# Kernel optimization log

Hardware: AMD Instinct MI355X
Metric: run time of the kernel (lower is better)

The kernel has to match this reference:

```python
import jax, jax.numpy as jnp
import numpy as np
import math

WS = 11
SIGMA = 1.5

def _gaussian_window(ws=WS, sigma=SIGMA):
    i = np.arange(ws)
    g = np.exp(-((i - ws // 2) ** 2) / (2.0 * sigma ** 2))
    g = (g / g.sum()).astype(np.float32)
    w2d = np.outer(g, g)  # [ws, ws]
    return jnp.asarray(w2d)

def _depthwise_conv(x, win2d):
    # x: [B, C, H, W]; win2d: [ws, ws]
    C = x.shape[1]
    kernel = jnp.broadcast_to(win2d[None, None], (C, 1, WS, WS)).astype(x.dtype)  # [C,1,ws,ws]
    return jax.lax.conv_general_dilated(
        x, kernel,
        window_strides=(1, 1),
        padding=[(WS // 2, WS // 2), (WS // 2, WS // 2)],
        dimension_numbers=("NCHW", "OIHW", "NCHW"),
        feature_group_count=C,
    )

def setup_inputs() -> dict:
    key = jax.random.key(0)
    k1, k2, k3 = jax.random.split(key, 3)
    B, C, H, W = 16, 3, 512, 512
    x = jax.random.uniform(k1, (B, C, H, W), dtype=jnp.float32)
    y = jax.random.uniform(k2, (B, C, H, W), dtype=jnp.float32)
    conf = jax.random.uniform(k3, (B, 1, H, W), dtype=jnp.float32)
    return {"x": x, "y": y, "conf": conf}

def reference(x, y, conf):
    win2d = _gaussian_window()
    mu_x = _depthwise_conv(x, win2d)
    mu_y = _depthwise_conv(y, win2d)
    mu_x2, mu_y2, mu_xy = mu_x * mu_x, mu_y * mu_y, mu_x * mu_y
    sigma_x2 = _depthwise_conv(x * x, win2d) - mu_x2
    sigma_y2 = _depthwise_conv(y * y, win2d) - mu_y2
    sigma_xy = _depthwise_conv(x * y, win2d) - mu_xy
    C1, C2 = 0.01 ** 2, 0.03 ** 2
    ssim = (2 * mu_xy + C1) * (2 * sigma_xy + C2) / ((mu_x2 + mu_y2 + C1) * (sigma_x2 + sigma_y2 + C2))
    loss_map = jnp.clip(1.0 - ssim, 0.0, 1.0)
    loss_map = loss_map * conf  # broadcast over channels
    return jnp.mean(loss_map)
```

## Files before the change

### kernel.cpp

```cpp
#include <hip/hip_runtime.h>
#include <cmath>

#define TW 32
#define SUB 32
#define NSUB 2
#define TH (SUB * NSUB)
#define HR (SUB + 10)
#define NT 256
#define IMG 512
#define SSIM_C1 1e-4f
#define SSIM_C2 9e-4f

struct GaussWin { float g[11]; };

typedef float v2f __attribute__((ext_vector_type(2)));

__device__ __forceinline__ v2f pk_fma(v2f a, v2f b, v2f c) {
    return __builtin_elementwise_fma(a, b, c);
}

__device__ __forceinline__ void h_pass_rows(const float* __restrict__ xp,
                                            const float* __restrict__ yp,
                                            int tx0, int gy0, int slot0, int nrows,
                                            const v2f* __restrict__ w2,
                                            float4* __restrict__ s_h, int tid) {
    constexpr int WI[11] = {0,1,2,3,4,5,4,3,2,1,0};
    if (tid < nrows * 4) {
        const int r = tid >> 2;
        const int cs = (tid & 3) * 8;
        const int gy = gy0 + r;
        const int slot = slot0 + r;
        const float* xrow = xp + gy * IMG;
        const float* yrow = yp + gy * IMG;
        const int c0 = tx0 + cs - 8;

        const bool fast = ((unsigned)gy < IMG) & ((unsigned)c0 <= (unsigned)(IMG - 24));

        float4 fx[6], fy[6];
        if (fast) {
            #pragma unroll
            for (int q = 0; q < 6; q++) {
                fx[q] = *(const float4*)(xrow + c0 + 4 * q);
                fy[q] = *(const float4*)(yrow + c0 + 4 * q);
            }
        } else {
            const bool rowok = ((unsigned)gy < IMG);
            #pragma unroll
            for (int q = 0; q < 6; q++) {
                int col = c0 + 4 * q;
                fx[q] = make_float4(0.f, 0.f, 0.f, 0.f);
                fy[q] = make_float4(0.f, 0.f, 0.f, 0.f);
                if (rowok && (unsigned)col <= (unsigned)(IMG - 4)) {
                    fx[q] = *(const float4*)(xrow + col);
                    fy[q] = *(const float4*)(yrow + col);
                }
            }
        }
        float vxa[24], vya[24];
        #pragma unroll
        for (int q = 0; q < 6; q++) {
            vxa[4*q+0]=fx[q].x; vxa[4*q+1]=fx[q].y; vxa[4*q+2]=fx[q].z; vxa[4*q+3]=fx[q].w;
            vya[4*q+0]=fy[q].x; vya[4*q+1]=fy[q].y; vya[4*q+2]=fy[q].z; vya[4*q+3]=fy[q].w;
        }

        v2f amu[8], a2[8];
        #pragma unroll
        for (int j = 0; j < 8; j++) { amu[j]=(v2f){0.f,0.f}; a2[j]=(v2f){0.f,0.f}; }
        #pragma unroll
        for (int k = 0; k < 18; k++) {
            float xv = vxa[k + 3], yv = vya[k + 3];
            v2f xy = (v2f){xv, yv};
            v2f p2 = xy * xy;
            v2f zw = (v2f){p2.x + p2.y, xv * yv};
            const int jlo = (k - 10 > 0) ? (k - 10) : 0;
            const int jhi = (k < 7) ? k : 7;
            #pragma unroll
            for (int j = jlo; j <= jhi; j++) {
                v2f w = w2[WI[k - j]];
                amu[j] = pk_fma(xy, w, amu[j]);
                a2[j]  = pk_fma(zw, w, a2[j]);
            }
        }
        const int quad = cs & 24;
        const int base0 = cs + 2 * (cs >> 3) + 5 * slot;
        #pragma unroll
        for (int j = 0; j < 8; j++) {
            int pc = quad | ((base0 + j) & 7);
            s_h[slot * TW + pc] = make_float4(amu[j].x, amu[j].y, a2[j].x, a2[j].y);
        }
    }
}

__launch_bounds__(NT, 4)
__global__ void ssim_tile_kernel(const float* __restrict__ x,
                                 const float* __restrict__ y,
                                 const float* __restrict__ conf,
                                 float* __restrict__ partials,
                                 float* __restrict__ out,
                                 int use_ws, float scale,
                                 GaussWin W) {
    __shared__ float4 s_h[HR * TW];
    __shared__ float  s_red[4];

    const int tid = threadIdx.x;
    const int plane = blockIdx.z;
    const int tx0 = blockIdx.x * TW;
    const int ty0 = blockIdx.y * TH;
    const float* xp = x + plane * (IMG * IMG);
    const float* yp = y + plane * (IMG * IMG);
    const int cbase = (plane / 3) * (IMG * IMG);

    constexpr int WI[11] = {0,1,2,3,4,5,4,3,2,1,0};
    v2f w2[6];
    #pragma unroll
    for (int i = 0; i < 6; i++) w2[i] = (v2f){W.g[i], W.g[i]};

    const int c   = tid & 31;
    const int r0c = (tid >> 5) * 4;
    const int cquad = c & 24;
    const int cb0 = c + 2 * (c >> 3) + 5 * r0c;
    int bidx[8];
    #pragma unroll
    for (int p = 0; p < 8; p++) {
        bidx[p] = r0c * TW + (cquad | ((cb0 + 5 * p) & 7));
    }

    float lsum = 0.f;
    float4 st0, st1;

    #pragma unroll
    for (int s = 0; s < NSUB; s++) {
        if (s == 0) {
            h_pass_rows(xp, yp, tx0, ty0 - 5, 0, HR, w2, s_h, tid);
        } else {
            __syncthreads();
            ((float4*)s_h)[tid] = st0;
            if (tid < 64) ((float4*)s_h)[256 + tid] = st1;
            h_pass_rows(xp, yp, tx0, ty0 + SUB * s + 5, 10, SUB, w2, s_h, tid);
        }

        float cf[4];
        #pragma unroll
        for (int j = 0; j < 4; j++) {
            cf[j] = conf[cbase + (ty0 + SUB * s + r0c + j) * IMG + tx0 + c];
        }
        __syncthreads();

        v2f amu[4], a2[4];
        #pragma unroll
        for (int j = 0; j < 4; j++) { amu[j]=(v2f){0.f,0.f}; a2[j]=(v2f){0.f,0.f}; }
        #pragma unroll
        for (int t = 0; t < 14; t++) {
            float4 h4 = s_h[bidx[t & 7] + t * TW];
            v2f hmu = (v2f){h4.x, h4.y};
            v2f h2  = (v2f){h4.z, h4.w};
            #pragma unroll
            for (int j = 0; j < 4; j++) {
                int k = t - j;
                if (k >= 0 && k <= 10) {
                    v2f w = w2[WI[k]];
                    amu[j] = pk_fma(hmu, w, amu[j]);
                    a2[j]  = pk_fma(h2, w, a2[j]);
                }
            }
        }

        if (s + 1 < NSUB) {
            st0 = ((const float4*)s_h)[32 * TW + tid];
            if (tid < 64) st1 = ((const float4*)s_h)[40 * TW + tid];
        }

        #pragma unroll
        for (int j = 0; j < 4; j++) {
            float mu_x = amu[j].x, mu_y = amu[j].y;
            v2f prod = amu[j] * amu[j];
            float mu_xy = mu_x * mu_y;
            float musq  = prod.x + prod.y;
            float sigsum = a2[j].x - musq;
            float sigxy  = a2[j].y - mu_xy;
            float num = fmaf(2.f, mu_xy, SSIM_C1) * fmaf(2.f, sigxy, SSIM_C2);
            float den = (musq + SSIM_C1) * (sigsum + SSIM_C2);
            float ssim = num * __builtin_amdgcn_rcpf(den);
            float loss = fminf(fmaxf(1.f - ssim, 0.f), 1.f);
            lsum = fmaf(loss, cf[j], lsum);
        }
    }

    #pragma unroll
    for (int off = 32; off; off >>= 1) lsum += __shfl_down(lsum, off, 64);
    if ((tid & 63) == 0) s_red[tid >> 6] = lsum;
    __syncthreads();
    if (tid == 0) {
        float t = s_red[0] + s_red[1] + s_red[2] + s_red[3];
        if (use_ws) {
            partials[blockIdx.x + gridDim.x * (blockIdx.y + gridDim.y * blockIdx.z)] = t;
        } else {
            atomicAdd(out, t * scale);
        }
    }
}

__global__ void reduce_kernel(const float* __restrict__ partials, int n,
                              float* __restrict__ out, float scale) {
    __shared__ float s_red[16];
    float s = 0.f;
    const float4* p4 = (const float4*)partials;
    const int n4 = n >> 2;
    for (int i = threadIdx.x; i < n4; i += 1024) {
        float4 v = p4[i];
        s += (v.x + v.y) + (v.z + v.w);
    }
    for (int i = (n4 << 2) + threadIdx.x; i < n; i += 1024) s += partials[i];
    #pragma unroll
    for (int off = 32; off; off >>= 1) s += __shfl_down(s, off, 64);
    if ((threadIdx.x & 63) == 0) s_red[threadIdx.x >> 6] = s;
    __syncthreads();
    if (threadIdx.x == 0) {
        float t = 0.f;
        #pragma unroll
        for (int i = 0; i < 16; i++) t += s_red[i];
        out[0] = t * scale;
    }
}

extern "C" void kernel_launch(void* const* d_in, const int* in_sizes, int n_in,
                              void* d_out, int out_size, void* d_ws, size_t ws_size,
                              hipStream_t stream) {
    const float* x    = (const float*)d_in[0];
    const float* y    = (const float*)d_in[1];
    const float* conf = (const float*)d_in[2];
    float* out = (float*)d_out;
    float* partials = (float*)d_ws;

    GaussWin W;
    {
        double gd[11], s = 0.0;
        for (int i = 0; i < 11; i++) { gd[i] = exp(-((i - 5) * (i - 5)) / 4.5); s += gd[i]; }
        for (int i = 0; i < 11; i++) W.g[i] = (float)(gd[i] / s);
    }

    const int B = 16, C = 3;
    const float scale = 1.0f / (float)(B * C * IMG * IMG);
    dim3 grid(IMG / TW, IMG / TH, B * C);
    const int nblocks = (IMG / TW) * (IMG / TH) * B * C;
    const int use_ws = (ws_size >= (size_t)nblocks * sizeof(float)) ? 1 : 0;

    if (!use_ws) {
        hipMemsetAsync(d_out, 0, sizeof(float), stream);
    }
    ssim_tile_kernel<<<grid, NT, 0, stream>>>(x, y, conf, partials, out, use_ws, scale, W);
    if (use_ws) {
        reduce_kernel<<<1, 1024, 0, stream>>>(partials, nblocks, out, scale);
    }
}
```

Measured before the change: 158.9 us.

## Double-buffer LDS and prefetch second sub-tile loads before first vertical pass

Splits the horizontal pass into separate load and compute phases and uses two LDS buffers. The global loads for the second sub-tile are issued before the first sub-tile's vertical pass and SSIM math, so their latency overlaps that work, and one barrier is dropped. In exchange, LDS use doubles and register pressure rises from keeping the prefetched data live, and the occupancy hint in launch bounds drops from 4 to 3.

```diff
diff --git a/kernel.cpp b/kernel.cpp
--- a/kernel.cpp
+++ b/kernel.cpp
@@ -3,9 +3,8 @@
 
 #define TW 32
 #define SUB 32
-#define NSUB 2
-#define TH (SUB * NSUB)
 #define HR (SUB + 10)
+#define BOFF (HR * TW)
 #define NT 256
 #define IMG 512
 #define SSIM_C1 1e-4f
@@ -19,24 +18,19 @@
     return __builtin_elementwise_fma(a, b, c);
 }
 
-__device__ __forceinline__ void h_pass_rows(const float* __restrict__ xp,
-                                            const float* __restrict__ yp,
-                                            int tx0, int gy0, int slot0, int nrows,
-                                            const v2f* __restrict__ w2,
-                                            float4* __restrict__ s_h, int tid) {
-    constexpr int WI[11] = {0,1,2,3,4,5,4,3,2,1,0};
+
+__device__ __forceinline__ void h_load(const float* __restrict__ xp,
+                                       const float* __restrict__ yp,
+                                       int tx0, int gy0, int nrows, int tid,
+                                       float4 fx[6], float4 fy[6]) {
     if (tid < nrows * 4) {
         const int r = tid >> 2;
         const int cs = (tid & 3) * 8;
         const int gy = gy0 + r;
-        const int slot = slot0 + r;
         const float* xrow = xp + gy * IMG;
         const float* yrow = yp + gy * IMG;
         const int c0 = tx0 + cs - 8;
-
         const bool fast = ((unsigned)gy < IMG) & ((unsigned)c0 <= (unsigned)(IMG - 24));
-
-        float4 fx[6], fy[6];
         if (fast) {
             #pragma unroll
             for (int q = 0; q < 6; q++) {
@@ -56,13 +50,24 @@
                 }
             }
         }
+    }
+}
+
+__device__ __forceinline__ void h_compute(int slot0, int nrows, int tid,
+                                          const v2f* __restrict__ w2,
+                                          const float4 fx[6], const float4 fy[6],
+                                          float4* __restrict__ buf) {
+    constexpr int WI[11] = {0,1,2,3,4,5,4,3,2,1,0};
+    if (tid < nrows * 4) {
+        const int r = tid >> 2;
+        const int cs = (tid & 3) * 8;
+        const int slot = slot0 + r;
         float vxa[24], vya[24];
         #pragma unroll
         for (int q = 0; q < 6; q++) {
             vxa[4*q+0]=fx[q].x; vxa[4*q+1]=fx[q].y; vxa[4*q+2]=fx[q].z; vxa[4*q+3]=fx[q].w;
             vya[4*q+0]=fy[q].x; vya[4*q+1]=fy[q].y; vya[4*q+2]=fy[q].z; vya[4*q+3]=fy[q].w;
         }
-
         v2f amu[8], a2[8];
         #pragma unroll
         for (int j = 0; j < 8; j++) { amu[j]=(v2f){0.f,0.f}; a2[j]=(v2f){0.f,0.f}; }
@@ -86,12 +91,12 @@
         #pragma unroll
         for (int j = 0; j < 8; j++) {
             int pc = quad | ((base0 + j) & 7);
-            s_h[slot * TW + pc] = make_float4(amu[j].x, amu[j].y, a2[j].x, a2[j].y);
-        }
-    }
-}
-
-__launch_bounds__(NT, 4)
+            buf[slot * TW + pc] = make_float4(amu[j].x, amu[j].y, a2[j].x, a2[j].y);
+        }
+    }
+}
+
+__launch_bounds__(NT, 3)
 __global__ void ssim_tile_kernel(const float* __restrict__ x,
                                  const float* __restrict__ y,
                                  const float* __restrict__ conf,
@@ -99,13 +104,13 @@
                                  float* __restrict__ out,
                                  int use_ws, float scale,
                                  GaussWin W) {
-    __shared__ float4 s_h[HR * TW];
+    __shared__ float4 s_h[2 * HR * TW];
     __shared__ float  s_red[4];
 
     const int tid = threadIdx.x;
     const int plane = blockIdx.z;
     const int tx0 = blockIdx.x * TW;
-    const int ty0 = blockIdx.y * TH;
+    const int ty0 = blockIdx.y * (2 * SUB);
     const float* xp = x + plane * (IMG * IMG);
     const float* yp = y + plane * (IMG * IMG);
     const int cbase = (plane / 3) * (IMG * IMG);
@@ -116,36 +121,38 @@
     for (int i = 0; i < 6; i++) w2[i] = (v2f){W.g[i], W.g[i]};
 
     const int c   = tid & 31;
-    const int r0c = (tid >> 5) * 4;
+    const int r0  = (tid >> 5) * 4;
     const int cquad = c & 24;
-    const int cb0 = c + 2 * (c >> 3) + 5 * r0c;
+    const int cb0 = c + 2 * (c >> 3) + 5 * r0;
     int bidx[8];
     #pragma unroll
     for (int p = 0; p < 8; p++) {
-        bidx[p] = r0c * TW + (cquad | ((cb0 + 5 * p) & 7));
+        bidx[p] = r0 * TW + (cquad | ((cb0 + 5 * p) & 7));
     }
 
     float lsum = 0.f;
-    float4 st0, st1;
-
-    #pragma unroll
-    for (int s = 0; s < NSUB; s++) {
-        if (s == 0) {
-            h_pass_rows(xp, yp, tx0, ty0 - 5, 0, HR, w2, s_h, tid);
-        } else {
-            __syncthreads();
-            ((float4*)s_h)[tid] = st0;
-            if (tid < 64) ((float4*)s_h)[256 + tid] = st1;
-            h_pass_rows(xp, yp, tx0, ty0 + SUB * s + 5, 10, SUB, w2, s_h, tid);
-        }
-
-        float cf[4];
-        #pragma unroll
-        for (int j = 0; j < 4; j++) {
-            cf[j] = conf[cbase + (ty0 + SUB * s + r0c + j) * IMG + tx0 + c];
-        }
-        __syncthreads();
-
+    float4 fx[6], fy[6];
+
+    h_load(xp, yp, tx0, ty0 - 5, HR, tid, fx, fy);
+    float cf0[4];
+    #pragma unroll
+    for (int j = 0; j < 4; j++) {
+        cf0[j] = conf[cbase + (ty0 + r0 + j) * IMG + tx0 + c];
+    }
+    h_compute(0, HR, tid, w2, fx, fy, s_h);
+    __syncthreads();
+
+    h_load(xp, yp, tx0, ty0 + SUB + 5, SUB, tid, fx, fy);
+    float cf1[4];
+    #pragma unroll
+    for (int j = 0; j < 4; j++) {
+        cf1[j] = conf[cbase + (ty0 + SUB + r0 + j) * IMG + tx0 + c];
+    }
+    float4 st0 = s_h[32 * TW + tid];
+    float4 st1;
+    if (tid < 64) st1 = s_h[40 * TW + tid];
+
+    {
         v2f amu[4], a2[4];
         #pragma unroll
         for (int j = 0; j < 4; j++) { amu[j]=(v2f){0.f,0.f}; a2[j]=(v2f){0.f,0.f}; }
@@ -164,12 +171,6 @@
                 }
             }
         }
-
-        if (s + 1 < NSUB) {
-            st0 = ((const float4*)s_h)[32 * TW + tid];
-            if (tid < 64) st1 = ((const float4*)s_h)[40 * TW + tid];
-        }
-
         #pragma unroll
         for (int j = 0; j < 4; j++) {
             float mu_x = amu[j].x, mu_y = amu[j].y;
@@ -182,7 +183,47 @@
             float den = (musq + SSIM_C1) * (sigsum + SSIM_C2);
             float ssim = num * __builtin_amdgcn_rcpf(den);
             float loss = fminf(fmaxf(1.f - ssim, 0.f), 1.f);
-            lsum = fmaf(loss, cf[j], lsum);
+            lsum = fmaf(loss, cf0[j], lsum);
+        }
+    }
+
+    s_h[BOFF + tid] = st0;
+    if (tid < 64) s_h[BOFF + 256 + tid] = st1;
+    h_compute(10, SUB, tid, w2, fx, fy, s_h + BOFF);
+    __syncthreads();
+
+    {
+        v2f amu[4], a2[4];
+        #pragma unroll
+        for (int j = 0; j < 4; j++) { amu[j]=(v2f){0.f,0.f}; a2[j]=(v2f){0.f,0.f}; }
+        #pragma unroll
+        for (int t = 0; t < 14; t++) {
+            float4 h4 = s_h[BOFF + bidx[t & 7] + t * TW];
+            v2f hmu = (v2f){h4.x, h4.y};
+            v2f h2  = (v2f){h4.z, h4.w};
+            #pragma unroll
+            for (int j = 0; j < 4; j++) {
+                int k = t - j;
+                if (k >= 0 && k <= 10) {
+                    v2f w = w2[WI[k]];
+                    amu[j] = pk_fma(hmu, w, amu[j]);
+                    a2[j]  = pk_fma(h2, w, a2[j]);
+                }
+            }
+        }
+        #pragma unroll
+        for (int j = 0; j < 4; j++) {
+            float mu_x = amu[j].x, mu_y = amu[j].y;
+            v2f prod = amu[j] * amu[j];
+            float mu_xy = mu_x * mu_y;
+            float musq  = prod.x + prod.y;
+            float sigsum = a2[j].x - musq;
+            float sigxy  = a2[j].y - mu_xy;
+            float num = fmaf(2.f, mu_xy, SSIM_C1) * fmaf(2.f, sigxy, SSIM_C2);
+            float den = (musq + SSIM_C1) * (sigsum + SSIM_C2);
+            float ssim = num * __builtin_amdgcn_rcpf(den);
+            float loss = fminf(fmaxf(1.f - ssim, 0.f), 1.f);
+            lsum = fmaf(loss, cf1[j], lsum);
         }
     }
 
@@ -241,8 +282,8 @@
 
     const int B = 16, C = 3;
     const float scale = 1.0f / (float)(B * C * IMG * IMG);
-    dim3 grid(IMG / TW, IMG / TH, B * C);
-    const int nblocks = (IMG / TW) * (IMG / TH) * B * C;
+    dim3 grid(IMG / TW, IMG / (2 * SUB), B * C);
+    const int nblocks = (IMG / TW) * (IMG / (2 * SUB)) * B * C;
     const int use_ws = (ws_size >= (size_t)nblocks * sizeof(float)) ? 1 : 0;
 
     if (!use_ws) {
```

New measurement: 167.9 us. 5.7% more time.
